# Performance work log

Hardware: AMD Instinct MI355X
Metric: run time of the kernel (lower is better)

Reference implementation:

```python
import jax, jax.numpy as jnp
import numpy as np
from jax import lax

B, T, F, C = 2, 249, 64, 256   # fixed by alpha/beta weight shapes in build()
K = 3                          # conv kernel size
FILT = 256                     # q/k conv filters (both blocks)
V = 256                        # v conv filters (both blocks)
OUT_CH = 64                    # conv2d_final filters (hardcoded)


def conv2d(x, w, b):
    # NHWC 'same' conv, stride 1, dilation 1
    return lax.conv_general_dilated(
        x, w, window_strides=(1, 1), padding='SAME',
        dimension_numbers=('NHWC', 'HWIO', 'NHWC')) + b


def attn_block(x, wq, bq, wk, bk, wv, bv):
    # x: [B, H, L, C]; attention over L per (batch, H) slice
    q = conv2d(x, wq, bq)          # [B,H,L,FILT]
    k = conv2d(x, wk, bk)          # [B,H,L,FILT]
    v = conv2d(x, wv, bv)          # [B,H,L,V]
    scores = jnp.einsum('bhqc,bhkc->bhqk', q, k)   # [B,H,L,L]
    dist = jax.nn.softmax(scores, axis=-1)
    return jnp.einsum('bhqk,bhkc->bhqc', dist, v)  # [B,H,L,V]


def setup_inputs() -> dict:
    key = jax.random.key(0)
    ks = jax.random.split(key, 18)
    s = 0.05
    d = {'x': jax.random.normal(ks[0], (B, T, F, C), jnp.float32)}
    names = ['wq_f', 'wk_f', 'wv_f', 'wq_t', 'wk_t', 'wv_t']
    outs = [FILT, FILT, V, FILT, FILT, V]
    for i, (n, o) in enumerate(zip(names, outs)):
        d[n] = jax.random.normal(ks[1 + i], (K, K, C, o), jnp.float32) * s
        d['b' + n[1:]] = jnp.zeros((o,), jnp.float32)
    d['w_final'] = jax.random.normal(ks[8], (K, K, V + V + C, OUT_CH), jnp.float32) * s
    d['b_final'] = jnp.zeros((OUT_CH,), jnp.float32)
    d['alpha'] = jax.random.uniform(ks[9], (B, T, F, V), jnp.float32, -0.05, 0.05)
    d['beta'] = jax.random.uniform(ks[10], (B, T, F, V), jnp.float32, -0.05, 0.05)
    return d


def reference(x, wq_f, bq_f, wk_f, bk_f, wv_f, bv_f,
              wq_t, bq_t, wk_t, bk_t, wv_t, bv_t,
              w_final, b_final, alpha, beta):
    # AFAB: transpose to [B,F,T,C], attend over time axis T
    xt = jnp.transpose(x, (0, 2, 1, 3))
    out_freq = attn_block(xt, wq_f, bq_f, wk_f, bk_f, wv_f, bv_f)
    out_freq = jnp.transpose(out_freq, (0, 2, 1, 3))  # back to [B,T,F,V]
    # ATAB: attend over frequency axis F directly on [B,T,F,C]
    out_time = attn_block(x, wq_t, bq_t, wk_t, bk_t, wv_t, bv_t)
    # learned elementwise gating + concat + final conv (concatenation=True path)
    fused = jnp.concatenate([alpha * out_freq, beta * out_time, x], axis=-1)
    return conv2d(fused, w_final, b_final)
```

## Files before the change

kernel.cpp:

```cpp
#include <hip/hip_runtime.h>


typedef _Float16 f16;
typedef _Float16 f16x8 __attribute__((ext_vector_type(8)));
typedef float    f32x4 __attribute__((ext_vector_type(4)));

#define B_   2
#define T_   249
#define F_   64
#define TP   251
#define FP   66
#define PIXB (T_*F_)
#define NPIX (B_*PIXB)
#define LPAD 256

static constexpr size_t FUSED_BYTES = (size_t)B_*TP*FP*768*2;
static constexpr size_t XPAD_BYTES  = (size_t)B_*TP*FP*256*2;
static constexpr size_t QF_BYTES    = (size_t)B_*64*LPAD*256*2;
static constexpr size_t QT_BYTES    = (size_t)B_*T_*64*256*2;
static constexpr size_t WT_BYTES    = (size_t)9*1536*256*2;
static constexpr size_t WFT_BYTES   = (size_t)9*64*768*2;

static constexpr size_t OFF_FUSED = 0;
static constexpr size_t OFF_XPAD  = OFF_FUSED + FUSED_BYTES;
static constexpr size_t OFF_QF    = OFF_XPAD  + XPAD_BYTES;
static constexpr size_t OFF_KF    = OFF_QF + QF_BYTES;
static constexpr size_t OFF_VF    = OFF_KF + QF_BYTES;
static constexpr size_t OFF_QT    = OFF_VF + QF_BYTES;
static constexpr size_t OFF_KT    = OFF_QT + QT_BYTES;
static constexpr size_t OFF_VT    = OFF_KT + QT_BYTES;
static constexpr size_t OFF_WT    = OFF_VT + QT_BYTES;
static constexpr size_t OFF_WFT   = OFF_WT + WT_BYTES;
static constexpr size_t OFF_BALL  = OFF_WFT + WFT_BYTES;
static constexpr size_t OFF_BF    = OFF_BALL + 1536*4;
static constexpr size_t WS_NEED   = OFF_BF + 64*4;

__device__ __forceinline__ f32x4 mfma16(f16x8 a, f16x8 b, f32x4 c) {
    return __builtin_amdgcn_mfma_f32_16x16x32_f16(a, b, c, 0, 0, 0);
}

__device__ __forceinline__ void gl_lds16(const void* g, void* l) {
    __builtin_amdgcn_global_load_lds(
        (const __attribute__((address_space(1))) unsigned int*)(unsigned long long)g,
        (__attribute__((address_space(3))) unsigned int*)(unsigned int)(unsigned long long)l,
        16, 0, 0);
}

__global__ __launch_bounds__(256) void prep_w(
    const float* __restrict__ wqf, const float* __restrict__ wkf, const float* __restrict__ wvf,
    const float* __restrict__ wqt, const float* __restrict__ wkt, const float* __restrict__ wvt,
    const float* __restrict__ wfin,
    const float* __restrict__ bqf, const float* __restrict__ bkf, const float* __restrict__ bvf,
    const float* __restrict__ bqt, const float* __restrict__ bkt, const float* __restrict__ bvt,
    const float* __restrict__ bfin,
    f16* __restrict__ wT, f16* __restrict__ wfT,
    float* __restrict__ biasAll, float* __restrict__ biasF)
{
    int idx = blockIdx.x*256 + threadIdx.x;
    if (idx < 9*1536*256) {
        int tap = idx / (1536*256);
        int r   = idx - tap*(1536*256);
        int n = r >> 8, c = r & 255;
        int dt = tap/3 - 1, df = tap%3 - 1;
        int blk = n >> 8, nl = n & 255;
        const float* w; int kh, kw;
        if (blk < 3) { w = (blk==0) ? wqf : (blk==1) ? wkf : wvf; kh = df+1; kw = dt+1; }
        else         { w = (blk==3) ? wqt : (blk==4) ? wkt : wvt; kh = dt+1; kw = df+1; }
        wT[idx] = (f16)w[((kh*3 + kw)*256 + c)*256 + nl];
    }
    if (idx < 9*64*768) {
        int tap = idx / (64*768);
        int r   = idx - tap*(64*768);
        int oc = r / 768, cin = r - oc*768;
        int dt = tap/3 - 1, df = tap%3 - 1;
        wfT[idx] = (f16)wfin[(((dt+1)*3 + (df+1))*768 + cin)*64 + oc];
    }
    if (idx < 1536) {
        int blk = idx >> 8, nl = idx & 255;
        const float* bb = (blk==0)?bqf:(blk==1)?bkf:(blk==2)?bvf:(blk==3)?bqt:(blk==4)?bkt:bvt;
        biasAll[idx] = bb[nl];
    }
    if (idx < 64) biasF[idx] = bfin[idx];
}

__global__ __launch_bounds__(256) void prep_x(
    const float* __restrict__ x, f16* __restrict__ xpad, f16* __restrict__ fused)
{
    int tid = blockIdx.x*256 + threadIdx.x;
    int pix = tid >> 5, c8 = (tid & 31)*8;
    int b = pix / PIXB; int r = pix - b*PIXB;
    int t = r >> 6, f = r & 63;
    const float* src = x + (size_t)pix*256 + c8;
    f16x8 v;
#pragma unroll
    for (int j = 0; j < 8; ++j) v[j] = (f16)src[j];
    size_t pp = (size_t)(b*TP + t + 1)*FP + (f + 1);
    *(f16x8*)(xpad + pp*256 + c8) = v;
    *(f16x8*)(fused + pp*768 + 512 + c8) = v;
}

__global__ __launch_bounds__(256) void conv_qkv(
    const f16* __restrict__ xpad, const f16* __restrict__ wT,
    const float* __restrict__ biasAll,
    f16* __restrict__ qf, f16* __restrict__ kf, f16* __restrict__ vf,
    f16* __restrict__ qt, f16* __restrict__ kt, f16* __restrict__ vt)
{
    __shared__ f16 ldsA[128*64];
    __shared__ f16 ldsB[128*64];
    const int l   = threadIdx.x & 63;
    const int wid = threadIdx.x >> 6;
    const int nt  = blockIdx.x;
    const int mt  = blockIdx.y;
    const int wm = wid >> 1, wn = wid & 1;

    int aBase[4], bBase[4];
#pragma unroll
    for (int i = 0; i < 4; ++i) {
        int row = wid*32 + i*8 + (l >> 3);
        int ch  = (l & 7) ^ (row & 7);
        int p = mt*128 + row;
        int b = p / PIXB; int r = p - b*PIXB;
        int t = r >> 6, f = r & 63;
        aBase[i] = ((b*TP + t + 1)*FP + (f + 1))*256 + ch*8;
        bBase[i] = (nt*128 + row)*256 + ch*8;
    }

    f32x4 acc[4][4];
#pragma unroll
    for (int mi = 0; mi < 4; ++mi)
#pragma unroll
        for (int ni = 0; ni < 4; ++ni) acc[mi][ni] = {0.f, 0.f, 0.f, 0.f};

    for (int tap = 0; tap < 9; ++tap) {
        const int dt = tap/3 - 1, df = tap%3 - 1;
        const int ash = (dt*FP + df)*256;
        const f16* wtap = wT + (size_t)tap*1536*256;
        for (int kc = 0; kc < 4; ++kc) {
            const int c0 = kc*64;
#pragma unroll
            for (int i = 0; i < 4; ++i) {
                gl_lds16(xpad + aBase[i] + ash + c0, ldsA + (wid*32 + i*8)*64);
                gl_lds16(wtap + bBase[i] + c0,       ldsB + (wid*32 + i*8)*64);
            }
            __syncthreads();
#pragma unroll
            for (int kk = 0; kk < 2; ++kk) {
                const int cch = kk*4 + (l >> 4);
                f16x8 af[4], bf[4];
#pragma unroll
                for (int mi = 0; mi < 4; ++mi) {
                    int row = wm*64 + mi*16 + (l & 15);
                    af[mi] = *(const f16x8*)(ldsA + row*64 + ((cch ^ (row & 7)) << 3));
                }
#pragma unroll
                for (int ni = 0; ni < 4; ++ni) {
                    int row = wn*64 + ni*16 + (l & 15);
                    bf[ni] = *(const f16x8*)(ldsB + row*64 + ((cch ^ (row & 7)) << 3));
                }
#pragma unroll
                for (int mi = 0; mi < 4; ++mi)
#pragma unroll
                    for (int ni = 0; ni < 4; ++ni)
                        acc[mi][ni] = mfma16(af[mi], bf[ni], acc[mi][ni]);
            }
            __syncthreads();
        }
    }

    const int buf = nt >> 1;
    f16* dst = (buf==0)?qf:(buf==1)?kf:(buf==2)?vf:(buf==3)?qt:(buf==4)?kt:vt;
#pragma unroll
    for (int mi = 0; mi < 4; ++mi) {
#pragma unroll
        for (int rg = 0; rg < 4; ++rg) {
            int row = wm*64 + mi*16 + (l >> 4)*4 + rg;
            int p = mt*128 + row;
            int b = p / PIXB; int r = p - b*PIXB;
            int t = r >> 6, f = r & 63;
#pragma unroll
            for (int ni = 0; ni < 4; ++ni) {
                int col = wn*64 + ni*16 + (l & 15);
                int ocg = nt*128 + col;
                int ocl = ocg & 255;
                float v = acc[mi][ni][rg] + biasAll[ocg];
                int off;
                if (buf < 2)       off = ((b*64 + f)*LPAD + t)*256 + ocl;
                else if (buf == 2) off = ((b*64 + f)*256 + ocl)*LPAD + t;
                else if (buf < 5)  off = ((b*T_ + t)*64 + f)*256 + ocl;
                else               off = ((b*T_ + t)*256 + ocl)*64 + f;
                dst[off] = (f16)v;
            }
        }
    }
}

__global__ __launch_bounds__(256) void attn_f(
    const f16* __restrict__ qf, const f16* __restrict__ kf, const f16* __restrict__ vf,
    const float* __restrict__ alpha, f16* __restrict__ fused)
{
    __shared__ f16 plds[4][16*256];
    const int l = threadIdx.x & 63;
    const int wid = threadIdx.x >> 6;
    const int head = blockIdx.x >> 2;
    const int qb = blockIdx.x & 3;
    const int b = head >> 6, f = head & 63;
    const f16* qh = qf + (size_t)head*LPAD*256;
    const f16* kh = kf + (size_t)head*LPAD*256;
    const f16* vh = vf + (size_t)head*256*LPAD;
    const int qr0 = qb*64 + wid*16;
    f16* pw = &plds[wid][0];

    f16x8 qa[8];
#pragma unroll
    for (int ks = 0; ks < 8; ++ks)
        qa[ks] = *(const f16x8*)(qh + (qr0 + (l & 15))*256 + ks*32 + (l >> 4)*8);

    f32x4 s[16];
#pragma unroll
    for (int nf = 0; nf < 16; ++nf) s[nf] = {0.f, 0.f, 0.f, 0.f};
#pragma unroll
    for (int ks = 0; ks < 8; ++ks)
#pragma unroll
        for (int nf = 0; nf < 16; ++nf) {
            f16x8 bf = *(const f16x8*)(kh + (nf*16 + (l & 15))*256 + ks*32 + (l >> 4)*8);
            s[nf] = mfma16(qa[ks], bf, s[nf]);
        }

    float inv[4];
#pragma unroll
    for (int rg = 0; rg < 4; ++rg) {
        float m = -1e30f;
#pragma unroll
        for (int nf = 0; nf < 16; ++nf)
            if (nf*16 + (l & 15) < T_) m = fmaxf(m, s[nf][rg]);
#pragma unroll
        for (int d = 1; d < 16; d <<= 1) m = fmaxf(m, __shfl_xor(m, d, 64));
        float sum = 0.f;
#pragma unroll
        for (int nf = 0; nf < 16; ++nf) {
            float p = (nf*16 + (l & 15) < T_) ? __expf(s[nf][rg] - m) : 0.f;
            s[nf][rg] = p;
            sum += p;
        }
#pragma unroll
        for (int d = 1; d < 16; d <<= 1) sum += __shfl_xor(sum, d, 64);
        inv[rg] = 1.f / sum;
    }

#pragma unroll
    for (int nf = 0; nf < 16; ++nf)
#pragma unroll
        for (int rg = 0; rg < 4; ++rg) {
            int row = (l >> 4)*4 + rg;
            int col = nf*16 + (l & 15);
            int byte = (row*512 + col*2) ^ ((row & 7) << 4);
            *(f16*)((char*)pw + byte) = (f16)s[nf][rg];
        }

    f32x4 o[16];
#pragma unroll
    for (int nf = 0; nf < 16; ++nf) o[nf] = {0.f, 0.f, 0.f, 0.f};
#pragma unroll
    for (int ks = 0; ks < 8; ++ks) {
        int row = l & 15;
        int cch = ks*4 + (l >> 4);
        int byte = row*512 + ((cch ^ (row & 7)) << 4);
        f16x8 pa = *(const f16x8*)((const char*)pw + byte);
#pragma unroll
        for (int nf = 0; nf < 16; ++nf) {
            f16x8 bf = *(const f16x8*)(vh + (nf*16 + (l & 15))*LPAD + ks*32 + (l >> 4)*8);
            o[nf] = mfma16(pa, bf, o[nf]);
        }
    }

#pragma unroll
    for (int rg = 0; rg < 4; ++rg) {
        int t = qr0 + (l >> 4)*4 + rg;
        if (t < T_) {
#pragma unroll
            for (int nf = 0; nf < 16; ++nf) {
                int c = nf*16 + (l & 15);
                float v = o[nf][rg] * inv[rg] * alpha[((size_t)(b*T_ + t)*64 + f)*256 + c];
                fused[((size_t)(b*TP + t + 1)*FP + (f + 1))*768 + c] = (f16)v;
            }
        }
    }
}

__global__ __launch_bounds__(256) void attn_t(
    const f16* __restrict__ qt, const f16* __restrict__ kt, const f16* __restrict__ vt,
    const float* __restrict__ beta, f16* __restrict__ fused)
{
    __shared__ f16 plds[4][16*64];
    const int l = threadIdx.x & 63;
    const int wid = threadIdx.x >> 6;
    const int head = blockIdx.x;
    const int b = head / T_, t = head - b*T_;
    const f16* qh = qt + (size_t)head*64*256;
    const f16* kh = kt + (size_t)head*64*256;
    const f16* vh = vt + (size_t)head*256*64;
    const int qr0 = wid*16;
    f16* pw = &plds[wid][0];

    f16x8 qa[8];
#pragma unroll
    for (int ks = 0; ks < 8; ++ks)
        qa[ks] = *(const f16x8*)(qh + (qr0 + (l & 15))*256 + ks*32 + (l >> 4)*8);

    f32x4 s[4];
#pragma unroll
    for (int nf = 0; nf < 4; ++nf) s[nf] = {0.f, 0.f, 0.f, 0.f};
#pragma unroll
    for (int ks = 0; ks < 8; ++ks)
#pragma unroll
        for (int nf = 0; nf < 4; ++nf) {
            f16x8 bf = *(const f16x8*)(kh + (nf*16 + (l & 15))*256 + ks*32 + (l >> 4)*8);
            s[nf] = mfma16(qa[ks], bf, s[nf]);
        }

    float inv[4];
#pragma unroll
    for (int rg = 0; rg < 4; ++rg) {
        float m = -1e30f;
#pragma unroll
        for (int nf = 0; nf < 4; ++nf) m = fmaxf(m, s[nf][rg]);
#pragma unroll
        for (int d = 1; d < 16; d <<= 1) m = fmaxf(m, __shfl_xor(m, d, 64));
        float sum = 0.f;
#pragma unroll
        for (int nf = 0; nf < 4; ++nf) {
            float p = __expf(s[nf][rg] - m);
            s[nf][rg] = p;
            sum += p;
        }
#pragma unroll
        for (int d = 1; d < 16; d <<= 1) sum += __shfl_xor(sum, d, 64);
        inv[rg] = 1.f / sum;
    }

#pragma unroll
    for (int nf = 0; nf < 4; ++nf)
#pragma unroll
        for (int rg = 0; rg < 4; ++rg) {
            int row = (l >> 4)*4 + rg;
            int col = nf*16 + (l & 15);
            int byte = (row*128 + col*2) ^ ((row & 7) << 4);
            *(f16*)((char*)pw + byte) = (f16)s[nf][rg];
        }

    f32x4 o[16];
#pragma unroll
    for (int nf = 0; nf < 16; ++nf) o[nf] = {0.f, 0.f, 0.f, 0.f};
#pragma unroll
    for (int ks = 0; ks < 2; ++ks) {
        int row = l & 15;
        int cch = ks*4 + (l >> 4);
        int byte = row*128 + ((cch ^ (row & 7)) << 4);
        f16x8 pa = *(const f16x8*)((const char*)pw + byte);
#pragma unroll
        for (int nf = 0; nf < 16; ++nf) {
            f16x8 bf = *(const f16x8*)(vh + (nf*16 + (l & 15))*64 + ks*32 + (l >> 4)*8);
            o[nf] = mfma16(pa, bf, o[nf]);
        }
    }

#pragma unroll
    for (int rg = 0; rg < 4; ++rg) {
        int fo = qr0 + (l >> 4)*4 + rg;
#pragma unroll
        for (int nf = 0; nf < 16; ++nf) {
            int c = nf*16 + (l & 15);
            float v = o[nf][rg] * inv[rg] * beta[((size_t)(b*T_ + t)*64 + fo)*256 + c];
            fused[((size_t)(b*TP + t + 1)*FP + (fo + 1))*768 + 256 + c] = (f16)v;
        }
    }
}

__global__ __launch_bounds__(256) void conv_final(
    const f16* __restrict__ fused, const f16* __restrict__ wfT,
    const float* __restrict__ biasF, float* __restrict__ out)
{
    __shared__ f16 ldsA[128*64];
    __shared__ f16 ldsB[64*64];
    const int l = threadIdx.x & 63;
    const int wid = threadIdx.x >> 6;
    const int mt = blockIdx.x;

    int aBase[4], bBase[2];
#pragma unroll
    for (int i = 0; i < 4; ++i) {
        int row = wid*32 + i*8 + (l >> 3);
        int ch  = (l & 7) ^ (row & 7);
        int p = mt*128 + row;
        int b = p / PIXB; int r = p - b*PIXB;
        int t = r >> 6, f = r & 63;
        aBase[i] = ((b*TP + t + 1)*FP + (f + 1))*768 + ch*8;
    }
#pragma unroll
    for (int i = 0; i < 2; ++i) {
        int row = wid*16 + i*8 + (l >> 3);
        int ch  = (l & 7) ^ (row & 7);
        bBase[i] = row*768 + ch*8;
    }

    f32x4 acc[2][4];
#pragma unroll
    for (int mi = 0; mi < 2; ++mi)
#pragma unroll
        for (int ni = 0; ni < 4; ++ni) acc[mi][ni] = {0.f, 0.f, 0.f, 0.f};

    for (int tap = 0; tap < 9; ++tap) {
        const int dt = tap/3 - 1, df = tap%3 - 1;
        const int ash = (dt*FP + df)*768;
        const f16* wt = wfT + (size_t)tap*64*768;
        for (int kc = 0; kc < 12; ++kc) {
            const int c0 = kc*64;
#pragma unroll
            for (int i = 0; i < 4; ++i)
                gl_lds16(fused + aBase[i] + ash + c0, ldsA + (wid*32 + i*8)*64);
#pragma unroll
            for (int i = 0; i < 2; ++i)
                gl_lds16(wt + bBase[i] + c0, ldsB + (wid*16 + i*8)*64);
            __syncthreads();
#pragma unroll
            for (int kk = 0; kk < 2; ++kk) {
                const int cch = kk*4 + (l >> 4);
                f16x8 af[2], bf[4];
#pragma unroll
                for (int mi = 0; mi < 2; ++mi) {
                    int row = wid*32 + mi*16 + (l & 15);
                    af[mi] = *(const f16x8*)(ldsA + row*64 + ((cch ^ (row & 7)) << 3));
                }
#pragma unroll
                for (int ni = 0; ni < 4; ++ni) {
                    int row = ni*16 + (l & 15);
                    bf[ni] = *(const f16x8*)(ldsB + row*64 + ((cch ^ (row & 7)) << 3));
                }
#pragma unroll
                for (int mi = 0; mi < 2; ++mi)
#pragma unroll
                    for (int ni = 0; ni < 4; ++ni)
                        acc[mi][ni] = mfma16(af[mi], bf[ni], acc[mi][ni]);
            }
            __syncthreads();
        }
    }

#pragma unroll
    for (int mi = 0; mi < 2; ++mi)
#pragma unroll
        for (int rg = 0; rg < 4; ++rg) {
            int row = wid*32 + mi*16 + (l >> 4)*4 + rg;
            int p = mt*128 + row;
#pragma unroll
            for (int ni = 0; ni < 4; ++ni) {
                int oc = ni*16 + (l & 15);
                out[(size_t)p*64 + oc] = acc[mi][ni][rg] + biasF[oc];
            }
        }
}

extern "C" void kernel_launch(void* const* d_in, const int* in_sizes, int n_in,
                              void* d_out, int out_size, void* d_ws, size_t ws_size,
                              hipStream_t stream) {
    (void)in_sizes; (void)n_in; (void)out_size;
    const float* x    = (const float*)d_in[0];
    const float* wqf  = (const float*)d_in[1];
    const float* bqf  = (const float*)d_in[2];
    const float* wkf  = (const float*)d_in[3];
    const float* bkf  = (const float*)d_in[4];
    const float* wvf  = (const float*)d_in[5];
    const float* bvf  = (const float*)d_in[6];
    const float* wqt  = (const float*)d_in[7];
    const float* bqt  = (const float*)d_in[8];
    const float* wkt  = (const float*)d_in[9];
    const float* bkt  = (const float*)d_in[10];
    const float* wvt  = (const float*)d_in[11];
    const float* bvt  = (const float*)d_in[12];
    const float* wfin = (const float*)d_in[13];
    const float* bfin = (const float*)d_in[14];
    const float* alpha= (const float*)d_in[15];
    const float* beta = (const float*)d_in[16];

    if (ws_size < WS_NEED) return;

    char* ws = (char*)d_ws;
    f16* fused  = (f16*)(ws + OFF_FUSED);
    f16* xpad   = (f16*)(ws + OFF_XPAD);
    f16* qf     = (f16*)(ws + OFF_QF);
    f16* kf     = (f16*)(ws + OFF_KF);
    f16* vf     = (f16*)(ws + OFF_VF);
    f16* qt     = (f16*)(ws + OFF_QT);
    f16* kt     = (f16*)(ws + OFF_KT);
    f16* vt     = (f16*)(ws + OFF_VT);
    f16* wT     = (f16*)(ws + OFF_WT);
    f16* wfT    = (f16*)(ws + OFF_WFT);
    float* bAll = (float*)(ws + OFF_BALL);
    float* bF   = (float*)(ws + OFF_BF);

    hipMemsetAsync(fused, 0, FUSED_BYTES, stream);
    hipMemsetAsync(xpad,  0, XPAD_BYTES,  stream);
    hipMemsetAsync(vf,    0, QF_BYTES,    stream);

    prep_w<<<dim3((9*1536*256 + 255)/256), dim3(256), 0, stream>>>(
        wqf, wkf, wvf, wqt, wkt, wvt, wfin,
        bqf, bkf, bvf, bqt, bkt, bvt, bfin, wT, wfT, bAll, bF);
    prep_x<<<dim3(NPIX*32/256), dim3(256), 0, stream>>>(x, xpad, fused);
    conv_qkv<<<dim3(12, 249), dim3(256), 0, stream>>>(xpad, wT, bAll, qf, kf, vf, qt, kt, vt);
    attn_f<<<dim3(512), dim3(256), 0, stream>>>(qf, kf, vf, alpha, fused);
    attn_t<<<dim3(498), dim3(256), 0, stream>>>(qt, kt, vt, beta, fused);
    conv_final<<<dim3(249), dim3(256), 0, stream>>>(fused, wfT, bF, (float*)d_out);
}
```

Before: 584.6 us.

## Restructure QKV conv GEMM with 128x256 tiles, triple-buffered LDS and XCD-aware remap

The QKV implicit-GEMM conv now uses 512-thread blocks computing 128x256 output tiles, with a K-step of 32 channels. A three-stage LDS ring buffer, explicit vmcnt waits, a single barrier per step and MFMA priority bumps overlap global-to-LDS loads with compute. Block IDs are remapped so that consecutive N-tiles of the same M-tile share an XCD, which improves L2 reuse of the activation tile. This trades more LDS and register pressure per block for fewer synchronisations and better latency hiding.

```diff
diff --git a/kernel.cpp b/kernel.cpp
--- a/kernel.cpp
+++ b/kernel.cpp
@@ -99,30 +99,47 @@
     *(f16x8*)(fused + pp*768 + 512 + c8) = v;
 }
 
-__global__ __launch_bounds__(256) void conv_qkv(
+__global__ __launch_bounds__(512, 4) void conv_qkv(
     const f16* __restrict__ xpad, const f16* __restrict__ wT,
     const float* __restrict__ biasAll,
     f16* __restrict__ qf, f16* __restrict__ kf, f16* __restrict__ vf,
-    f16* __restrict__ qt, f16* __restrict__ kt, f16* __restrict__ vt)
+    f16* __restrict__ qt, f16* __restrict__ kt_, f16* __restrict__ vt)
 {
-    __shared__ f16 ldsA[128*64];
-    __shared__ f16 ldsB[128*64];
+    __shared__ f16 smem[3*12288];
+
+    const int nwgq = 186, nwgr = 6;
+    int xcd = blockIdx.x & 7, lin = blockIdx.x >> 3;
+    int wg = (xcd < nwgr ? xcd*(nwgq+1) : nwgr*(nwgq+1) + (xcd-nwgr)*nwgq) + lin;
+    const int mt = wg / 6;
+    const int nt = wg - mt*6;
+
     const int l   = threadIdx.x & 63;
     const int wid = threadIdx.x >> 6;
-    const int nt  = blockIdx.x;
-    const int mt  = blockIdx.y;
-    const int wm = wid >> 1, wn = wid & 1;
-
-    int aBase[4], bBase[4];
-#pragma unroll
-    for (int i = 0; i < 4; ++i) {
-        int row = wid*32 + i*8 + (l >> 3);
-        int ch  = (l & 7) ^ (row & 7);
-        int p = mt*128 + row;
-        int b = p / PIXB; int r = p - b*PIXB;
-        int t = r >> 6, f = r & 63;
-        aBase[i] = ((b*TP + t + 1)*FP + (f + 1))*256 + ch*8;
-        bBase[i] = (nt*128 + row)*256 + ch*8;
+    const int wm = wid >> 2, wn = wid & 3;
+
+    int rowA = wid*16 + (l >> 2);
+    {
+    }
+    int pA = mt*128 + rowA;
+    int bA = pA / PIXB; int rA = pA - bA*PIXB;
+    int tA = rA >> 6, fA = rA & 63;
+    const int chA = (l & 3) ^ ((rowA >> 1) & 3);
+    const int aSrc = ((bA*TP + tA + 1)*FP + (fA + 1))*256 + chA*8;
+    const int rowB = wid*16 + (l >> 2);
+    const int chB = (l & 3) ^ ((rowB >> 1) & 3);
+    const int bSrc0 = (nt*256 + rowB)*256 + chB*8;
+    const int bSrc1 = bSrc0 + 128*256;
+
+    int aOff[4], bOff[4];
+#pragma unroll
+    for (int mi = 0; mi < 4; ++mi) {
+        int row = wm*64 + mi*16 + (l & 15);
+        aOff[mi] = row*32 + ((((l >> 4)) ^ ((row >> 1) & 3)) << 3);
+    }
+#pragma unroll
+    for (int ni = 0; ni < 4; ++ni) {
+        int row = wn*64 + ni*16 + (l & 15);
+        bOff[ni] = 4096 + row*32 + ((((l >> 4)) ^ ((row >> 1) & 3)) << 3);
     }
 
     f32x4 acc[4][4];
@@ -131,44 +148,51 @@
 #pragma unroll
         for (int ni = 0; ni < 4; ++ni) acc[mi][ni] = {0.f, 0.f, 0.f, 0.f};
 
-    for (int tap = 0; tap < 9; ++tap) {
-        const int dt = tap/3 - 1, df = tap%3 - 1;
-        const int ash = (dt*FP + df)*256;
-        const f16* wtap = wT + (size_t)tap*1536*256;
-        for (int kc = 0; kc < 4; ++kc) {
-            const int c0 = kc*64;
-#pragma unroll
-            for (int i = 0; i < 4; ++i) {
-                gl_lds16(xpad + aBase[i] + ash + c0, ldsA + (wid*32 + i*8)*64);
-                gl_lds16(wtap + bBase[i] + c0,       ldsB + (wid*32 + i*8)*64);
-            }
-            __syncthreads();
-#pragma unroll
-            for (int kk = 0; kk < 2; ++kk) {
-                const int cch = kk*4 + (l >> 4);
-                f16x8 af[4], bf[4];
-#pragma unroll
-                for (int mi = 0; mi < 4; ++mi) {
-                    int row = wm*64 + mi*16 + (l & 15);
-                    af[mi] = *(const f16x8*)(ldsA + row*64 + ((cch ^ (row & 7)) << 3));
-                }
-#pragma unroll
-                for (int ni = 0; ni < 4; ++ni) {
-                    int row = wn*64 + ni*16 + (l & 15);
-                    bf[ni] = *(const f16x8*)(ldsB + row*64 + ((cch ^ (row & 7)) << 3));
-                }
-#pragma unroll
-                for (int mi = 0; mi < 4; ++mi)
-#pragma unroll
-                    for (int ni = 0; ni < 4; ++ni)
-                        acc[mi][ni] = mfma16(af[mi], bf[ni], acc[mi][ni]);
-            }
-            __syncthreads();
-        }
-    }
-
-    const int buf = nt >> 1;
-    f16* dst = (buf==0)?qf:(buf==1)?kf:(buf==2)?vf:(buf==3)?qt:(buf==4)?kt:vt;
+#define QKV_STAGE(KN, NB) do {                                                 \
+        int tap_ = (KN) >> 3, kc_ = (KN) & 7;                                  \
+        int dt_ = tap_/3 - 1, df_ = tap_ - (tap_/3)*3 - 1;                     \
+        int ash_ = (dt_*FP + df_)*256 + kc_*32;                                \
+        int bsh_ = tap_*(1536*256) + kc_*32;                                   \
+        gl_lds16(xpad + aSrc + ash_, smem + (NB)*12288 + wid*512);             \
+        gl_lds16(wT + bSrc0 + bsh_,  smem + (NB)*12288 + 4096 + wid*512);      \
+        gl_lds16(wT + bSrc1 + bsh_,  smem + (NB)*12288 + 8192 + wid*512);      \
+    } while (0)
+
+#define QKV_STEP(KT, CUR, NB) do {                                             \
+        if ((KT) < 71) asm volatile("s_waitcnt vmcnt(3)" ::: "memory");        \
+        else           asm volatile("s_waitcnt vmcnt(0)" ::: "memory");        \
+        __builtin_amdgcn_s_barrier();                                          \
+        __builtin_amdgcn_sched_barrier(0);                                     \
+        if ((KT) + 2 < 72) { QKV_STAGE((KT) + 2, NB); }                        \
+        {                                                                      \
+            const f16* bp_ = smem + (CUR)*12288;                               \
+            f16x8 af_[4], bf_[4];                                              \
+            _Pragma("unroll")                                                  \
+            for (int mi = 0; mi < 4; ++mi) af_[mi] = *(const f16x8*)(bp_ + aOff[mi]); \
+            _Pragma("unroll")                                                  \
+            for (int ni = 0; ni < 4; ++ni) bf_[ni] = *(const f16x8*)(bp_ + bOff[ni]); \
+            __builtin_amdgcn_s_setprio(1);                                     \
+            _Pragma("unroll")                                                  \
+            for (int mi = 0; mi < 4; ++mi)                                     \
+                _Pragma("unroll")                                              \
+                for (int ni = 0; ni < 4; ++ni)                                 \
+                    acc[mi][ni] = mfma16(af_[mi], bf_[ni], acc[mi][ni]);       \
+            __builtin_amdgcn_s_setprio(0);                                     \
+        }                                                                      \
+    } while (0)
+
+    QKV_STAGE(0, 0);
+    QKV_STAGE(1, 1);
+
+    for (int kt = 0; kt < 72; kt += 3) {
+        QKV_STEP(kt + 0, 0, 2);
+        QKV_STEP(kt + 1, 1, 0);
+        QKV_STEP(kt + 2, 2, 1);
+    }
+#undef QKV_STEP
+#undef QKV_STAGE
+
+    f16* dst = (nt==0)?qf:(nt==1)?kf:(nt==2)?vf:(nt==3)?qt:(nt==4)?kt_:vt;
 #pragma unroll
     for (int mi = 0; mi < 4; ++mi) {
 #pragma unroll
@@ -180,14 +204,13 @@
 #pragma unroll
             for (int ni = 0; ni < 4; ++ni) {
                 int col = wn*64 + ni*16 + (l & 15);
-                int ocg = nt*128 + col;
-                int ocl = ocg & 255;
+                int ocg = nt*256 + col;
                 float v = acc[mi][ni][rg] + biasAll[ocg];
                 int off;
-                if (buf < 2)       off = ((b*64 + f)*LPAD + t)*256 + ocl;
-                else if (buf == 2) off = ((b*64 + f)*256 + ocl)*LPAD + t;
-                else if (buf < 5)  off = ((b*T_ + t)*64 + f)*256 + ocl;
-                else               off = ((b*T_ + t)*256 + ocl)*64 + f;
+                if (nt < 2)       off = ((b*64 + f)*LPAD + t)*256 + col;
+                else if (nt == 2) off = ((b*64 + f)*256 + col)*LPAD + t;
+                else if (nt < 5)  off = ((b*T_ + t)*64 + f)*256 + col;
+                else              off = ((b*T_ + t)*256 + col)*64 + f;
                 dst[off] = (f16)v;
             }
         }
@@ -506,7 +529,7 @@
         wqf, wkf, wvf, wqt, wkt, wvt, wfin,
         bqf, bkf, bvf, bqt, bkt, bvt, bfin, wT, wfT, bAll, bF);
     prep_x<<<dim3(NPIX*32/256), dim3(256), 0, stream>>>(x, xpad, fused);
-    conv_qkv<<<dim3(12, 249), dim3(256), 0, stream>>>(xpad, wT, bAll, qf, kf, vf, qt, kt, vt);
+    conv_qkv<<<dim3(1494), dim3(512), 0, stream>>>(xpad, wT, bAll, qf, kf, vf, qt, kt, vt);
     attn_f<<<dim3(512), dim3(256), 0, stream>>>(qf, kf, vf, alpha, fused);
     attn_t<<<dim3(498), dim3(256), 0, stream>>>(qt, kt, vt, beta, fused);
     conv_final<<<dim3(249), dim3(256), 0, stream>>>(fused, wfT, bF, (float*)d_out);
```

Result: slower. 637.5 us (+9.1%).

## Widen conv_qkv N-tile with XCD-aware remap; retile conv_final for more blocks

Applied to the files above, without the earlier changes.

conv_qkv now computes a 128x256 output tile per block, up from 128x128. This halves the number of times each A (input) tile is reloaded. Blocks come from a flat 1D grid remapped so neighbouring M-tiles stay on the same XCD, which should improve L2 reuse of weights and activations. conv_final now uses 64-pixel M tiles with a 128-wide K chunk, giving 498 blocks instead of 249 for better CU occupancy. The trade-off is more accumulator registers and LDS in conv_qkv, plus doubled B-tile loads per block in conv_final.

```diff
diff --git a/kernel.cpp b/kernel.cpp
--- a/kernel.cpp
+++ b/kernel.cpp
@@ -99,37 +99,60 @@
     *(f16x8*)(fused + pp*768 + 512 + c8) = v;
 }
 
-__global__ __launch_bounds__(256) void conv_qkv(
+__global__ __launch_bounds__(256, 2) void conv_qkv(
     const f16* __restrict__ xpad, const f16* __restrict__ wT,
     const float* __restrict__ biasAll,
     f16* __restrict__ qf, f16* __restrict__ kf, f16* __restrict__ vf,
-    f16* __restrict__ qt, f16* __restrict__ kt, f16* __restrict__ vt)
+    f16* __restrict__ qt, f16* __restrict__ kt_, f16* __restrict__ vt)
 {
     __shared__ f16 ldsA[128*64];
-    __shared__ f16 ldsB[128*64];
+    __shared__ f16 ldsB[256*64];
+
+    const int nwgq = 186, nwgr = 6;
+    int xcd = blockIdx.x & 7, lin = blockIdx.x >> 3;
+    int wg = (xcd < nwgr ? xcd*(nwgq+1) : nwgr*(nwgq+1) + (xcd-nwgr)*nwgq) + lin;
+    const int mt = wg / 6;
+    const int nt = wg - mt*6;
+
     const int l   = threadIdx.x & 63;
     const int wid = threadIdx.x >> 6;
-    const int nt  = blockIdx.x;
-    const int mt  = blockIdx.y;
     const int wm = wid >> 1, wn = wid & 1;
 
-    int aBase[4], bBase[4];
+    int aSrc[4];
 #pragma unroll
     for (int i = 0; i < 4; ++i) {
-        int row = wid*32 + i*8 + (l >> 3);
+        int row = i*32 + wid*8 + (l >> 3);
         int ch  = (l & 7) ^ (row & 7);
         int p = mt*128 + row;
         int b = p / PIXB; int r = p - b*PIXB;
         int t = r >> 6, f = r & 63;
-        aBase[i] = ((b*TP + t + 1)*FP + (f + 1))*256 + ch*8;
-        bBase[i] = (nt*128 + row)*256 + ch*8;
-    }
-
-    f32x4 acc[4][4];
+        aSrc[i] = ((b*TP + t + 1)*FP + (f + 1))*256 + ch*8;
+    }
+    int bSrc[8];
+#pragma unroll
+    for (int j = 0; j < 8; ++j) {
+        int row = j*32 + wid*8 + (l >> 3);
+        int ch  = (l & 7) ^ (row & 7);
+        bSrc[j] = (nt*256 + row)*256 + ch*8;
+    }
+
+    int aRow[4], aSw[4], bRow[8], bSw[8];
+#pragma unroll
+    for (int mi = 0; mi < 4; ++mi) {
+        int row = wm*64 + mi*16 + (l & 15);
+        aRow[mi] = row*64; aSw[mi] = row & 7;
+    }
+#pragma unroll
+    for (int ni = 0; ni < 8; ++ni) {
+        int row = wn*128 + ni*16 + (l & 15);
+        bRow[ni] = row*64; bSw[ni] = row & 7;
+    }
+
+    f32x4 acc[4][8];
 #pragma unroll
     for (int mi = 0; mi < 4; ++mi)
 #pragma unroll
-        for (int ni = 0; ni < 4; ++ni) acc[mi][ni] = {0.f, 0.f, 0.f, 0.f};
+        for (int ni = 0; ni < 8; ++ni) acc[mi][ni] = {0.f, 0.f, 0.f, 0.f};
 
     for (int tap = 0; tap < 9; ++tap) {
         const int dt = tap/3 - 1, df = tap%3 - 1;
@@ -138,37 +161,33 @@
         for (int kc = 0; kc < 4; ++kc) {
             const int c0 = kc*64;
 #pragma unroll
-            for (int i = 0; i < 4; ++i) {
-                gl_lds16(xpad + aBase[i] + ash + c0, ldsA + (wid*32 + i*8)*64);
-                gl_lds16(wtap + bBase[i] + c0,       ldsB + (wid*32 + i*8)*64);
-            }
+            for (int i = 0; i < 4; ++i)
+                gl_lds16(xpad + aSrc[i] + ash + c0, ldsA + (i*32 + wid*8)*64);
+#pragma unroll
+            for (int j = 0; j < 8; ++j)
+                gl_lds16(wtap + bSrc[j] + c0, ldsB + (j*32 + wid*8)*64);
             __syncthreads();
 #pragma unroll
             for (int kk = 0; kk < 2; ++kk) {
                 const int cch = kk*4 + (l >> 4);
-                f16x8 af[4], bf[4];
-#pragma unroll
-                for (int mi = 0; mi < 4; ++mi) {
-                    int row = wm*64 + mi*16 + (l & 15);
-                    af[mi] = *(const f16x8*)(ldsA + row*64 + ((cch ^ (row & 7)) << 3));
-                }
-#pragma unroll
-                for (int ni = 0; ni < 4; ++ni) {
-                    int row = wn*64 + ni*16 + (l & 15);
-                    bf[ni] = *(const f16x8*)(ldsB + row*64 + ((cch ^ (row & 7)) << 3));
-                }
+                f16x8 af[4], bf[8];
 #pragma unroll
                 for (int mi = 0; mi < 4; ++mi)
-#pragma unroll
-                    for (int ni = 0; ni < 4; ++ni)
+                    af[mi] = *(const f16x8*)(ldsA + aRow[mi] + ((cch ^ aSw[mi]) << 3));
+#pragma unroll
+                for (int ni = 0; ni < 8; ++ni)
+                    bf[ni] = *(const f16x8*)(ldsB + bRow[ni] + ((cch ^ bSw[ni]) << 3));
+#pragma unroll
+                for (int mi = 0; mi < 4; ++mi)
+#pragma unroll
+                    for (int ni = 0; ni < 8; ++ni)
                         acc[mi][ni] = mfma16(af[mi], bf[ni], acc[mi][ni]);
             }
             __syncthreads();
         }
     }
 
-    const int buf = nt >> 1;
-    f16* dst = (buf==0)?qf:(buf==1)?kf:(buf==2)?vf:(buf==3)?qt:(buf==4)?kt:vt;
+    f16* dst = (nt==0)?qf:(nt==1)?kf:(nt==2)?vf:(nt==3)?qt:(nt==4)?kt_:vt;
 #pragma unroll
     for (int mi = 0; mi < 4; ++mi) {
 #pragma unroll
@@ -178,16 +197,14 @@
             int b = p / PIXB; int r = p - b*PIXB;
             int t = r >> 6, f = r & 63;
 #pragma unroll
-            for (int ni = 0; ni < 4; ++ni) {
-                int col = wn*64 + ni*16 + (l & 15);
-                int ocg = nt*128 + col;
-                int ocl = ocg & 255;
-                float v = acc[mi][ni][rg] + biasAll[ocg];
+            for (int ni = 0; ni < 8; ++ni) {
+                int col = wn*128 + ni*16 + (l & 15);
+                float v = acc[mi][ni][rg] + biasAll[nt*256 + col];
                 int off;
-                if (buf < 2)       off = ((b*64 + f)*LPAD + t)*256 + ocl;
-                else if (buf == 2) off = ((b*64 + f)*256 + ocl)*LPAD + t;
-                else if (buf < 5)  off = ((b*T_ + t)*64 + f)*256 + ocl;
-                else               off = ((b*T_ + t)*256 + ocl)*64 + f;
+                if (nt < 2)       off = ((b*64 + f)*LPAD + t)*256 + col;
+                else if (nt == 2) off = ((b*64 + f)*256 + col)*LPAD + t;
+                else if (nt < 5)  off = ((b*T_ + t)*64 + f)*256 + col;
+                else              off = ((b*T_ + t)*256 + col)*64 + f;
                 dst[off] = (f16)v;
             }
         }
@@ -376,88 +393,80 @@
     }
 }
 
-__global__ __launch_bounds__(256) void conv_final(
+__global__ __launch_bounds__(256, 3) void conv_final(
     const f16* __restrict__ fused, const f16* __restrict__ wfT,
     const float* __restrict__ biasF, float* __restrict__ out)
 {
-    __shared__ f16 ldsA[128*64];
-    __shared__ f16 ldsB[64*64];
+    __shared__ f16 ldsA[64*128];
+    __shared__ f16 ldsB[64*128];
     const int l = threadIdx.x & 63;
     const int wid = threadIdx.x >> 6;
     const int mt = blockIdx.x;
-
-    int aBase[4], bBase[2];
+    const int b = mt / T_, t = mt - b*T_;
+
+    int aSrc[4], bSrc[4];
 #pragma unroll
     for (int i = 0; i < 4; ++i) {
-        int row = wid*32 + i*8 + (l >> 3);
-        int ch  = (l & 7) ^ (row & 7);
-        int p = mt*128 + row;
-        int b = p / PIXB; int r = p - b*PIXB;
-        int t = r >> 6, f = r & 63;
-        aBase[i] = ((b*TP + t + 1)*FP + (f + 1))*768 + ch*8;
-    }
-#pragma unroll
-    for (int i = 0; i < 2; ++i) {
-        int row = wid*16 + i*8 + (l >> 3);
-        int ch  = (l & 7) ^ (row & 7);
-        bBase[i] = row*768 + ch*8;
-    }
-
-    f32x4 acc[2][4];
-#pragma unroll
-    for (int mi = 0; mi < 2; ++mi)
-#pragma unroll
-        for (int ni = 0; ni < 4; ++ni) acc[mi][ni] = {0.f, 0.f, 0.f, 0.f};
+        int row = i*16 + wid*4 + (l >> 4);
+        int ch  = (l & 15) ^ (row & 7);
+        aSrc[i] = ((b*TP + t + 1)*FP + (row + 1))*768 + ch*8;
+        bSrc[i] = row*768 + ch*8;
+    }
+
+    int aRowOff, aSwz;
+    {
+        int row = wid*16 + (l & 15);
+        aRowOff = row*128; aSwz = row & 7;
+    }
+    int bRow[4], bSw[4];
+#pragma unroll
+    for (int ni = 0; ni < 4; ++ni) {
+        int row = ni*16 + (l & 15);
+        bRow[ni] = row*128; bSw[ni] = row & 7;
+    }
+
+    f32x4 acc[4];
+#pragma unroll
+    for (int ni = 0; ni < 4; ++ni) acc[ni] = {0.f, 0.f, 0.f, 0.f};
 
     for (int tap = 0; tap < 9; ++tap) {
         const int dt = tap/3 - 1, df = tap%3 - 1;
         const int ash = (dt*FP + df)*768;
         const f16* wt = wfT + (size_t)tap*64*768;
-        for (int kc = 0; kc < 12; ++kc) {
-            const int c0 = kc*64;
-#pragma unroll
-            for (int i = 0; i < 4; ++i)
-                gl_lds16(fused + aBase[i] + ash + c0, ldsA + (wid*32 + i*8)*64);
-#pragma unroll
-            for (int i = 0; i < 2; ++i)
-                gl_lds16(wt + bBase[i] + c0, ldsB + (wid*16 + i*8)*64);
-            __syncthreads();
-#pragma unroll
-            for (int kk = 0; kk < 2; ++kk) {
-                const int cch = kk*4 + (l >> 4);
-                f16x8 af[2], bf[4];
-#pragma unroll
-                for (int mi = 0; mi < 2; ++mi) {
-                    int row = wid*32 + mi*16 + (l & 15);
-                    af[mi] = *(const f16x8*)(ldsA + row*64 + ((cch ^ (row & 7)) << 3));
-                }
-#pragma unroll
-                for (int ni = 0; ni < 4; ++ni) {
-                    int row = ni*16 + (l & 15);
-                    bf[ni] = *(const f16x8*)(ldsB + row*64 + ((cch ^ (row & 7)) << 3));
-                }
-#pragma unroll
-                for (int mi = 0; mi < 2; ++mi)
-#pragma unroll
-                    for (int ni = 0; ni < 4; ++ni)
-                        acc[mi][ni] = mfma16(af[mi], bf[ni], acc[mi][ni]);
+        for (int kc = 0; kc < 6; ++kc) {
+            const int c0 = kc*128;
+#pragma unroll
+            for (int i = 0; i < 4; ++i) {
+                gl_lds16(fused + aSrc[i] + ash + c0, ldsA + (i*16 + wid*4)*128);
+                gl_lds16(wt + bSrc[i] + c0,          ldsB + (i*16 + wid*4)*128);
             }
             __syncthreads();
-        }
-    }
-
-#pragma unroll
-    for (int mi = 0; mi < 2; ++mi)
-#pragma unroll
-        for (int rg = 0; rg < 4; ++rg) {
-            int row = wid*32 + mi*16 + (l >> 4)*4 + rg;
-            int p = mt*128 + row;
-#pragma unroll
-            for (int ni = 0; ni < 4; ++ni) {
-                int oc = ni*16 + (l & 15);
-                out[(size_t)p*64 + oc] = acc[mi][ni][rg] + biasF[oc];
+#pragma unroll
+            for (int kk = 0; kk < 4; ++kk) {
+                const int cch = kk*4 + (l >> 4);
+                f16x8 af = *(const f16x8*)(ldsA + aRowOff + ((cch ^ aSwz) << 3));
+                f16x8 bf[4];
+#pragma unroll
+                for (int ni = 0; ni < 4; ++ni)
+                    bf[ni] = *(const f16x8*)(ldsB + bRow[ni] + ((cch ^ bSw[ni]) << 3));
+#pragma unroll
+                for (int ni = 0; ni < 4; ++ni)
+                    acc[ni] = mfma16(af, bf[ni], acc[ni]);
             }
-        }
+            __syncthreads();
+        }
+    }
+
+#pragma unroll
+    for (int rg = 0; rg < 4; ++rg) {
+        int f = wid*16 + (l >> 4)*4 + rg;
+        int p = mt*64 + f;
+#pragma unroll
+        for (int ni = 0; ni < 4; ++ni) {
+            int oc = ni*16 + (l & 15);
+            out[(size_t)p*64 + oc] = acc[ni][rg] + biasF[oc];
+        }
+    }
 }
 
 extern "C" void kernel_launch(void* const* d_in, const int* in_sizes, int n_in,
@@ -506,8 +515,8 @@
         wqf, wkf, wvf, wqt, wkt, wvt, wfin,
         bqf, bkf, bvf, bqt, bkt, bvt, bfin, wT, wfT, bAll, bF);
     prep_x<<<dim3(NPIX*32/256), dim3(256), 0, stream>>>(x, xpad, fused);
-    conv_qkv<<<dim3(12, 249), dim3(256), 0, stream>>>(xpad, wT, bAll, qf, kf, vf, qt, kt, vt);
+    conv_qkv<<<dim3(1494), dim3(256), 0, stream>>>(xpad, wT, bAll, qf, kf, vf, qt, kt, vt);
     attn_f<<<dim3(512), dim3(256), 0, stream>>>(qf, kf, vf, alpha, fused);
     attn_t<<<dim3(498), dim3(256), 0, stream>>>(qt, kt, vt, beta, fused);
-    conv_final<<<dim3(249), dim3(256), 0, stream>>>(fused, wfT, bF, (float*)d_out);
-}
+    conv_final<<<dim3(498), dim3(256), 0, stream>>>(fused, wfT, bF, (float*)d_out);
+}
```

Result: no change. 587.2 us (+0.4%).
